# Optimization experiments

Measured on AMD Instinct MI355X. Metric: run time of the kernel, lower is better.

## Reference

```python
import jax, jax.numpy as jnp
import numpy as np

B, H, N, DH = 4096, 4, 1024, 256  # batch, heads, codes per head, per-head dim
DECAY, EPS, COMMIT = 0.99, 1e-5, 0.25


def setup_inputs() -> dict:
    key = jax.random.key(0)
    k1, k2, k3, k4 = jax.random.split(key, 4)
    return {
        "inputs": jax.random.normal(k1, (B, 1, H * DH), dtype=jnp.float32),
        "emb_w": jax.random.normal(k2, (H, N, DH), dtype=jnp.float32),
        "ema_w": jax.random.normal(k3, (H, N, DH), dtype=jnp.float32),
        "cluster_size": jnp.zeros((H, N), dtype=jnp.float32),
        "trans_w": jax.random.normal(k4, (H, N, N), dtype=jnp.float32) * 0.03,
    }


def reference(inputs, emb_w, ema_w, cluster_size, trans_w):
    sg = jax.lax.stop_gradient
    x = inputs[:, 0, :].reshape(B, H, DH)  # split heads
    quant, codes = [], []
    prev_probs = None
    for h in range(H):
        xi = x[:, h]                       # [B, DH]
        w = emb_w[h]                       # [N, DH]
        # squared euclidean distances [B, N]
        d = (jnp.sum(xi * xi, axis=1, keepdims=True)
             + jnp.sum(w * w, axis=1)
             - 2.0 * xi @ w.T)
        logits = -sg(d)
        if prev_probs is not None:  # transition prior from previous head (detached)
            logits = logits + sg(prev_probs @ trans_w[h].T)
        probs = jax.nn.softmax(logits, axis=-1)
        prev_probs = probs
        # EMA codebook update (training mode)
        cs = cluster_size[h] * DECAY + (1.0 - DECAY) * jnp.sum(probs, axis=0)
        n = jnp.sum(cs)
        cs = (cs + EPS) / (n + N * EPS) * n
        dw = probs.T @ xi                  # [N, DH]
        ew = ema_w[h] * DECAY + (1.0 - DECAY) * dw
        new_w = ew / cs[:, None]           # updated codebook used for quantization
        codes.append(jnp.argmax(probs, axis=-1))
        quant.append(probs @ sg(new_w))    # soft-EM quantization, detached codebook
    quantized = jnp.stack(quant, axis=1).reshape(inputs.shape)  # [B,1,H*DH]
    q_loss = jnp.mean((quantized - sg(inputs)) ** 2, axis=(-1, -2))
    e_loss = jnp.mean((sg(quantized) - inputs) ** 2, axis=(-1, -2))
    loss = COMMIT * e_loss + q_loss        # [B]
    quantized = inputs + sg(quantized - inputs)  # straight-through
    vq_codes = jnp.stack(codes, axis=1)    # [B, H]
    return loss, quantized, vq_codes
```

## Files before the change

### kernel.cpp

```cpp
#include <hip/hip_runtime.h>
#include <hip/hip_bf16.h>
#include <math.h>

#define BB 4096
#define HH 4
#define NN 1024
#define DHD 256
#define XLD 1024
#define DECAY 0.99f
#define OMD 0.01f
#define EPSV 1e-5f

typedef __attribute__((ext_vector_type(8))) short bf16x8;
typedef __attribute__((ext_vector_type(4))) float f32x4;
typedef unsigned short u16;

#define MFMA(a, b, c) __builtin_amdgcn_mfma_f32_16x16x32_bf16((a), (b), (c), 0, 0, 0)

static __device__ __forceinline__ u16 f2bf(float x) {
    union { __hip_bfloat16 b; u16 u; } c; c.b = __float2bfloat16(x); return c.u;
}
static __device__ __forceinline__ float bf2f(u16 u) {
    union { __hip_bfloat16 b; u16 u; } c; c.u = u; return __bfloat162float(c.b);
}
static __device__ __forceinline__ void split3(float x, u16& h, u16& m, u16& l) {
    h = f2bf(x);
    float r = x - bf2f(h);
    m = f2bf(r);
    float r2 = r - bf2f(m);
    l = f2bf(r2);
}

__global__ __launch_bounds__(256) void k_prep_x(const float* __restrict__ in,
        u16* __restrict__ xh2, u16* __restrict__ xm2, u16* __restrict__ xl2,
        u16* __restrict__ xth, u16* __restrict__ xtl) {
    __shared__ float T[64][68];
    const int t = threadIdx.x;
    const int c0 = blockIdx.x * 64, i0 = blockIdx.y * 64;
#pragma unroll
    for (int rep = 0; rep < 4; rep++) {
        int id = t + 256 * rep;
        int row = id >> 4, c4 = (id & 15) * 4;
        float4 v = *(const float4*)(in + (size_t)(i0 + row) * XLD + c0 + c4);
        *(float4*)&T[row][c4] = v;
        float xs[4] = {v.x, v.y, v.z, v.w};
        u16 h4[4], m4[4], l4[4];
#pragma unroll
        for (int e = 0; e < 4; e++) split3(2.f * xs[e], h4[e], m4[e], l4[e]);
        size_t o = (size_t)(i0 + row) * XLD + c0 + c4;
        *(ushort4*)(xh2 + o) = make_ushort4(h4[0], h4[1], h4[2], h4[3]);
        *(ushort4*)(xm2 + o) = make_ushort4(m4[0], m4[1], m4[2], m4[3]);
        *(ushort4*)(xl2 + o) = make_ushort4(l4[0], l4[1], l4[2], l4[3]);
    }
    __syncthreads();
    const int or_ = t >> 2, oc = (t & 3) * 16;
    bf16x8 h0, h1, l0, l1;
#pragma unroll
    for (int e = 0; e < 8; e++) {
        float x = T[oc + e][or_];
        u16 h = f2bf(x);
        h0[e] = (short)h; l0[e] = (short)f2bf(x - bf2f(h));
    }
#pragma unroll
    for (int e = 0; e < 8; e++) {
        float x = T[oc + 8 + e][or_];
        u16 h = f2bf(x);
        h1[e] = (short)h; l1[e] = (short)f2bf(x - bf2f(h));
    }
    size_t o = (size_t)(c0 + or_) * BB + i0 + oc;
    *(bf16x8*)(xth + o) = h0;
    *(bf16x8*)(xth + o + 8) = h1;
    *(bf16x8*)(xtl + o) = l0;
    *(bf16x8*)(xtl + o + 8) = l1;
}

__global__ __launch_bounds__(256) void k_prep_w(const float* __restrict__ w,
        u16* __restrict__ wh, u16* __restrict__ wm, u16* __restrict__ wl) {
    size_t id = ((size_t)blockIdx.x * 256 + threadIdx.x) * 4;
    float4 v = *(const float4*)(w + id);
    float xs[4] = {v.x, v.y, v.z, v.w};
    u16 h4[4], m4[4], l4[4];
#pragma unroll
    for (int e = 0; e < 4; e++) split3(xs[e], h4[e], m4[e], l4[e]);
    *(ushort4*)(wh + id) = make_ushort4(h4[0], h4[1], h4[2], h4[3]);
    *(ushort4*)(wm + id) = make_ushort4(m4[0], m4[1], m4[2], m4[3]);
    *(ushort4*)(wl + id) = make_ushort4(l4[0], l4[1], l4[2], l4[3]);
}

__global__ __launch_bounds__(256) void k_prep_t(const float* __restrict__ w,
        u16* __restrict__ th, u16* __restrict__ tl) {
    size_t id = ((size_t)blockIdx.x * 256 + threadIdx.x) * 4;
    float4 v = *(const float4*)(w + id);
    float xs[4] = {v.x, v.y, v.z, v.w};
    u16 h4[4], l4[4];
#pragma unroll
    for (int e = 0; e < 4; e++) {
        u16 h = f2bf(xs[e]);
        h4[e] = h;
        l4[e] = f2bf(xs[e] - bf2f(h));
    }
    *(ushort4*)(th + id) = make_ushort4(h4[0], h4[1], h4[2], h4[3]);
    *(ushort4*)(tl + id) = make_ushort4(l4[0], l4[1], l4[2], l4[3]);
}

__global__ __launch_bounds__(256) void k_wsq(const float* __restrict__ emb,
                                             float* __restrict__ wsq) {
    int wave = threadIdx.x >> 6;
    int lane = threadIdx.x & 63;
    int row  = blockIdx.x * 4 + wave;
    const float* w = emb + (size_t)row * DHD;
    float4 v = *(const float4*)(w + lane * 4);
    float s = v.x * v.x + v.y * v.y + v.z * v.z + v.w * v.w;
    for (int off = 32; off; off >>= 1) s += __shfl_down(s, off);
    if (lane == 0) wsq[row] = s;
}

template <int HASPREV>
__global__ __launch_bounds__(256) void k_logits_mfma(
        const u16* __restrict__ Xh, const u16* __restrict__ Xm, const u16* __restrict__ Xl,
        const u16* __restrict__ Wh, const u16* __restrict__ Wm, const u16* __restrict__ Wl,
        const float* __restrict__ wsq,
        const u16* __restrict__ Ph, const u16* __restrict__ Pl,
        const u16* __restrict__ Th, const u16* __restrict__ Tl,
        float* __restrict__ L) {
    __shared__ u16 Ah[64 * 40], Am[64 * 40], Al[64 * 40];
    __shared__ u16 Bh[64 * 40], Bm[64 * 40], Bl[64 * 40];
    const int t = threadIdx.x;
    const int lane = t & 63, wid = t >> 6;
    const int wmi = wid >> 1, wn = wid & 1;
    const int q = lane >> 4, mr = lane & 15;
    const int j0 = blockIdx.x * 64, i0 = blockIdx.y * 64;
    const int ar = t >> 2, ac = (t & 3) * 8;

    f32x4 zero = {0.f, 0.f, 0.f, 0.f};
    f32x4 s[2][2], acc2[2][2];
#pragma unroll
    for (int mt = 0; mt < 2; mt++)
#pragma unroll
        for (int nt = 0; nt < 2; nt++) { s[mt][nt] = zero; acc2[mt][nt] = zero; }

    for (int kb = 0; kb < DHD; kb += 32) {
        bf16x8 a0h = *(const bf16x8*)(Xh + (size_t)(i0 + ar) * XLD + kb + ac);
        bf16x8 a0m = *(const bf16x8*)(Xm + (size_t)(i0 + ar) * XLD + kb + ac);
        bf16x8 a0l = *(const bf16x8*)(Xl + (size_t)(i0 + ar) * XLD + kb + ac);
        bf16x8 b0h = *(const bf16x8*)(Wh + (size_t)(j0 + ar) * DHD + kb + ac);
        bf16x8 b0m = *(const bf16x8*)(Wm + (size_t)(j0 + ar) * DHD + kb + ac);
        bf16x8 b0l = *(const bf16x8*)(Wl + (size_t)(j0 + ar) * DHD + kb + ac);
        __syncthreads();
        *(bf16x8*)&Ah[ar * 40 + ac] = a0h;
        *(bf16x8*)&Am[ar * 40 + ac] = a0m;
        *(bf16x8*)&Al[ar * 40 + ac] = a0l;
        *(bf16x8*)&Bh[ar * 40 + ac] = b0h;
        *(bf16x8*)&Bm[ar * 40 + ac] = b0m;
        *(bf16x8*)&Bl[ar * 40 + ac] = b0l;
        __syncthreads();
        bf16x8 afh[2], afm[2], afl[2], bfh[2], bfm[2], bfl[2];
#pragma unroll
        for (int mt = 0; mt < 2; mt++) {
            int row = (wmi * 32 + mt * 16 + mr) * 40 + q * 8;
            afh[mt] = *(const bf16x8*)&Ah[row];
            afm[mt] = *(const bf16x8*)&Am[row];
            afl[mt] = *(const bf16x8*)&Al[row];
        }
#pragma unroll
        for (int nt = 0; nt < 2; nt++) {
            int row = (wn * 32 + nt * 16 + mr) * 40 + q * 8;
            bfh[nt] = *(const bf16x8*)&Bh[row];
            bfm[nt] = *(const bf16x8*)&Bm[row];
            bfl[nt] = *(const bf16x8*)&Bl[row];
        }
#pragma unroll
        for (int mt = 0; mt < 2; mt++)
#pragma unroll
            for (int nt = 0; nt < 2; nt++) {
                f32x4 fresh = MFMA(afh[mt], bfh[nt], zero);
                s[mt][nt] += fresh;
                acc2[mt][nt] = MFMA(afh[mt], bfm[nt], acc2[mt][nt]);
                acc2[mt][nt] = MFMA(afm[mt], bfh[nt], acc2[mt][nt]);
                acc2[mt][nt] = MFMA(afh[mt], bfl[nt], acc2[mt][nt]);
                acc2[mt][nt] = MFMA(afm[mt], bfm[nt], acc2[mt][nt]);
                acc2[mt][nt] = MFMA(afl[mt], bfh[nt], acc2[mt][nt]);
            }
    }

    if (HASPREV) {
        for (int kb = 0; kb < NN; kb += 32) {
            bf16x8 a0h = *(const bf16x8*)(Ph + (size_t)(i0 + ar) * NN + kb + ac);
            bf16x8 a0l = *(const bf16x8*)(Pl + (size_t)(i0 + ar) * NN + kb + ac);
            bf16x8 b0h = *(const bf16x8*)(Th + (size_t)(j0 + ar) * NN + kb + ac);
            bf16x8 b0l = *(const bf16x8*)(Tl + (size_t)(j0 + ar) * NN + kb + ac);
            __syncthreads();
            *(bf16x8*)&Ah[ar * 40 + ac] = a0h;
            *(bf16x8*)&Al[ar * 40 + ac] = a0l;
            *(bf16x8*)&Bh[ar * 40 + ac] = b0h;
            *(bf16x8*)&Bl[ar * 40 + ac] = b0l;
            __syncthreads();
            bf16x8 afh[2], afl[2], bfh[2], bfl[2];
#pragma unroll
            for (int mt = 0; mt < 2; mt++) {
                int row = (wmi * 32 + mt * 16 + mr) * 40 + q * 8;
                afh[mt] = *(const bf16x8*)&Ah[row];
                afl[mt] = *(const bf16x8*)&Al[row];
            }
#pragma unroll
            for (int nt = 0; nt < 2; nt++) {
                int row = (wn * 32 + nt * 16 + mr) * 40 + q * 8;
                bfh[nt] = *(const bf16x8*)&Bh[row];
                bfl[nt] = *(const bf16x8*)&Bl[row];
            }
#pragma unroll
            for (int mt = 0; mt < 2; mt++)
#pragma unroll
                for (int nt = 0; nt < 2; nt++) {
                    acc2[mt][nt] = MFMA(afh[mt], bfh[nt], acc2[mt][nt]);
                    acc2[mt][nt] = MFMA(afh[mt], bfl[nt], acc2[mt][nt]);
                    acc2[mt][nt] = MFMA(afl[mt], bfh[nt], acc2[mt][nt]);
                }
        }
    }

    float wq[2];
#pragma unroll
    for (int nt = 0; nt < 2; nt++) wq[nt] = wsq[j0 + wn * 32 + nt * 16 + mr];
#pragma unroll
    for (int mt = 0; mt < 2; mt++)
#pragma unroll
        for (int nt = 0; nt < 2; nt++)
#pragma unroll
            for (int r = 0; r < 4; r++) {
                int gi = i0 + wmi * 32 + mt * 16 + q * 4 + r;
                int gj = j0 + wn * 32 + nt * 16 + mr;
// ... 42 lines not shown
    for (int ss = 128; ss; ss >>= 1) {
        if (t < ss) smax[t] += smax[t + ss];
        __syncthreads();
    }
    float inv = 1.0f / smax[0];
#pragma unroll
    for (int q4 = 0; q4 < 4; q4++) {
        float pv = v[q4] * inv;
        u16 hb = f2bf(pv);
        Ph[(size_t)i * NN + q4 * 256 + t] = hb;
        Pl[(size_t)i * NN + q4 * 256 + t] = f2bf(pv - bf2f(hb));
    }
    if (t == 0) codes[(size_t)i * HH + h] = (float)code;
}

__global__ __launch_bounds__(256) void k_transposeP(const u16* __restrict__ Ph,
        const u16* __restrict__ Pl, u16* __restrict__ PTh, u16* __restrict__ PTl) {
    __shared__ u16 U[64][72];
    const int t = threadIdx.x;
    const int j0 = blockIdx.x * 64, i0 = blockIdx.y * 64;
    for (int pass = 0; pass < 2; pass++) {
        const u16* src = pass ? Pl : Ph;
        u16* dst = pass ? PTl : PTh;
        if (pass) __syncthreads();
#pragma unroll
        for (int rep = 0; rep < 2; rep++) {
            int id = t + 256 * rep;
            int row = id >> 3, c8 = (id & 7) * 8;
            *(bf16x8*)&U[row][c8] = *(const bf16x8*)(src + (size_t)(i0 + row) * NN + j0 + c8);
        }
        __syncthreads();
        int or_ = t >> 2, oc = (t & 3) * 16;
        bf16x8 v0, v1;
#pragma unroll
        for (int e = 0; e < 8; e++) v0[e] = (short)U[oc + e][or_];
#pragma unroll
        for (int e = 0; e < 8; e++) v1[e] = (short)U[oc + 8 + e][or_];
        size_t o = (size_t)(j0 + or_) * BB + i0 + oc;
        *(bf16x8*)(dst + o) = v0;
        *(bf16x8*)(dst + o + 8) = v1;
    }
}

__global__ __launch_bounds__(256) void k_colsum(const u16* __restrict__ Ph,
                                                const u16* __restrict__ Pl,
                                                float* __restrict__ colsum) {
    int j  = blockIdx.x * 256 + threadIdx.x;
    int i0 = blockIdx.y * 256;
    float s = 0.f;
    for (int i = i0; i < i0 + 256; i++)
        s += bf2f(Ph[(size_t)i * NN + j]) + bf2f(Pl[(size_t)i * NN + j]);
    atomicAdd(&colsum[j], s);
}

__global__ __launch_bounds__(1024) void k_cs(const float* __restrict__ cluster_size,
                                             const float* __restrict__ colsum,
                                             float* __restrict__ csn, int h) {
    __shared__ float red[1024];
    int j = threadIdx.x;
    float cs = cluster_size[h * NN + j] * DECAY + OMD * colsum[j];
    red[j] = cs;
    __syncthreads();
    for (int s = 512; s; s >>= 1) {
        if (j < s) red[j] += red[j + s];
        __syncthreads();
    }
    float n = red[0];
    csn[j] = (cs + EPSV) / (n + NN * EPSV) * n;
}

__global__ __launch_bounds__(256) void k_dw(
        const u16* __restrict__ PTh, const u16* __restrict__ PTl,
        const u16* __restrict__ XTh, const u16* __restrict__ XTl,
        float* __restrict__ partial) {
    __shared__ u16 Ah[64 * 40], Al[64 * 40], Bh[64 * 40], Bl[64 * 40];
    const int t = threadIdx.x;
    const int lane = t & 63, wid = t >> 6;
    const int wmi = wid >> 1, wn = wid & 1;
    const int q = lane >> 4, mr = lane & 15;
    const int kd0 = blockIdx.x * 64, j0 = blockIdx.y * 64;
    const int ibeg = blockIdx.z * 256;
    const int ar = t >> 2, ac = (t & 3) * 8;

    f32x4 zero = {0.f, 0.f, 0.f, 0.f};
    f32x4 acc[2][2];
#pragma unroll
    for (int mt = 0; mt < 2; mt++)
#pragma unroll
        for (int nt = 0; nt < 2; nt++) acc[mt][nt] = zero;

    for (int ib = ibeg; ib < ibeg + 256; ib += 32) {
        bf16x8 a0h = *(const bf16x8*)(PTh + (size_t)(j0 + ar) * BB + ib + ac);
        bf16x8 a0l = *(const bf16x8*)(PTl + (size_t)(j0 + ar) * BB + ib + ac);
        bf16x8 b0h = *(const bf16x8*)(XTh + (size_t)(kd0 + ar) * BB + ib + ac);
        bf16x8 b0l = *(const bf16x8*)(XTl + (size_t)(kd0 + ar) * BB + ib + ac);
        __syncthreads();
        *(bf16x8*)&Ah[ar * 40 + ac] = a0h;
        *(bf16x8*)&Al[ar * 40 + ac] = a0l;
        *(bf16x8*)&Bh[ar * 40 + ac] = b0h;
        *(bf16x8*)&Bl[ar * 40 + ac] = b0l;
        __syncthreads();
        bf16x8 afh[2], afl[2], bfh[2], bfl[2];
#pragma unroll
        for (int mt = 0; mt < 2; mt++) {
            int row = (wmi * 32 + mt * 16 + mr) * 40 + q * 8;
            afh[mt] = *(const bf16x8*)&Ah[row];
            afl[mt] = *(const bf16x8*)&Al[row];
        }
#pragma unroll
        for (int nt = 0; nt < 2; nt++) {
            int row = (wn * 32 + nt * 16 + mr) * 40 + q * 8;
            bfh[nt] = *(const bf16x8*)&Bh[row];
            bfl[nt] = *(const bf16x8*)&Bl[row];
        }
#pragma unroll
        for (int mt = 0; mt < 2; mt++)
#pragma unroll
            for (int nt = 0; nt < 2; nt++) {
                acc[mt][nt] = MFMA(afh[mt], bfh[nt], acc[mt][nt]);
                acc[mt][nt] = MFMA(afh[mt], bfl[nt], acc[mt][nt]);
                acc[mt][nt] = MFMA(afl[mt], bfh[nt], acc[mt][nt]);
            }
    }
#pragma unroll
    for (int mt = 0; mt < 2; mt++)
#pragma unroll
        for (int nt = 0; nt < 2; nt++)
#pragma unroll
            for (int r = 0; r < 4; r++) {
                int gj = j0 + wmi * 32 + mt * 16 + q * 4 + r;
                int gk = kd0 + wn * 32 + nt * 16 + mr;
                atomicAdd(&partial[(size_t)gj * DHD + gk], acc[mt][nt][r]);
            }
}

__global__ __launch_bounds__(256) void k_neww_ep(const float* __restrict__ partial,
        const float* __restrict__ ema, const float* __restrict__ csn,
        u16* __restrict__ NWh, u16* __restrict__ NWl) {
    __shared__ float T[64][68];
    const int t = threadIdx.x;
    const int j0 = blockIdx.x * 64, kd0 = blockIdx.y * 64;
#pragma unroll
    for (int rep = 0; rep < 4; rep++) {
        int id = t + 256 * rep;
        int jr = id >> 4, c4 = (id & 15) * 4;
        float4 pp = *(const float4*)(partial + (size_t)(j0 + jr) * DHD + kd0 + c4);
        float4 ee = *(const float4*)(ema + (size_t)(j0 + jr) * DHD + kd0 + c4);
        float ic = 1.0f / csn[j0 + jr];
        float4 v;
        v.x = (ee.x * DECAY + OMD * pp.x) * ic;
        v.y = (ee.y * DECAY + OMD * pp.y) * ic;
        v.z = (ee.z * DECAY + OMD * pp.z) * ic;
        v.w = (ee.w * DECAY + OMD * pp.w) * ic;
        *(float4*)&T[jr][c4] = v;
    }
    __syncthreads();
    const int or_ = t >> 2, oc = (t & 3) * 16;
    bf16x8 h0, h1, l0, l1;
#pragma unroll
    for (int e = 0; e < 8; e++) {
        float x = T[oc + e][or_];
        u16 h = f2bf(x);
        h0[e] = (short)h; l0[e] = (short)f2bf(x - bf2f(h));
    }
#pragma unroll
    for (int e = 0; e < 8; e++) {
        float x = T[oc + 8 + e][or_];
        u16 h = f2bf(x);
        h1[e] = (short)h; l1[e] = (short)f2bf(x - bf2f(h));
    }
    size_t o = (size_t)(kd0 + or_) * NN + j0 + oc;
    *(bf16x8*)(NWh + o) = h0;
    *(bf16x8*)(NWh + o + 8) = h1;
    *(bf16x8*)(NWl + o) = l0;
    *(bf16x8*)(NWl + o + 8) = l1;
}

__global__ __launch_bounds__(256) void k_quant(
        const u16* __restrict__ Ph, const u16* __restrict__ Pl,
        const u16* __restrict__ NWh, const u16* __restrict__ NWl,
        float* __restrict__ outq, int h) {
    __shared__ u16 Ah[64 * 40], Al[64 * 40], Bh[64 * 40], Bl[64 * 40];
    const int t = threadIdx.x;
    const int lane = t & 63, wid = t >> 6;
    const int wmi = wid >> 1, wn = wid & 1;
    const int q = lane >> 4, mr = lane & 15;
    const int kd0 = blockIdx.x * 64, i0 = blockIdx.y * 64;
    const int jbeg = blockIdx.z * 256;
    const int ar = t >> 2, ac = (t & 3) * 8;

    f32x4 zero = {0.f, 0.f, 0.f, 0.f};
    f32x4 acc[2][2];
#pragma unroll
    for (int mt = 0; mt < 2; mt++)
#pragma unroll
        for (int nt = 0; nt < 2; nt++) acc[mt][nt] = zero;

    for (int jb = jbeg; jb < jbeg + 256; jb += 32) {
        bf16x8 a0h = *(const bf16x8*)(Ph + (size_t)(i0 + ar) * NN + jb + ac);
        bf16x8 a0l = *(const bf16x8*)(Pl + (size_t)(i0 + ar) * NN + jb + ac);
        bf16x8 b0h = *(const bf16x8*)(NWh + (size_t)(kd0 + ar) * NN + jb + ac);
        bf16x8 b0l = *(const bf16x8*)(NWl + (size_t)(kd0 + ar) * NN + jb + ac);
        __syncthreads();
        *(bf16x8*)&Ah[ar * 40 + ac] = a0h;
        *(bf16x8*)&Al[ar * 40 + ac] = a0l;
        *(bf16x8*)&Bh[ar * 40 + ac] = b0h;
        *(bf16x8*)&Bl[ar * 40 + ac] = b0l;
        __syncthreads();
        bf16x8 afh[2], afl[2], bfh[2], bfl[2];
#pragma unroll
        for (int mt = 0; mt < 2; mt++) {
            int row = (wmi * 32 + mt * 16 + mr) * 40 + q * 8;
            afh[mt] = *(const bf16x8*)&Ah[row];
            afl[mt] = *(const bf16x8*)&Al[row];
        }
#pragma unroll
        for (int nt = 0; nt < 2; nt++) {
            int row = (wn * 32 + nt * 16 + mr) * 40 + q * 8;
            bfh[nt] = *(const bf16x8*)&Bh[row];
            bfl[nt] = *(const bf16x8*)&Bl[row];
        }
#pragma unroll
        for (int mt = 0; mt < 2; mt++)
#pragma unroll
            for (int nt = 0; nt < 2; nt++) {
                acc[mt][nt] = MFMA(afh[mt], bfh[nt], acc[mt][nt]);
                acc[mt][nt] = MFMA(afh[mt], bfl[nt], acc[mt][nt]);
                acc[mt][nt] = MFMA(afl[mt], bfh[nt], acc[mt][nt]);
            }
    }
#pragma unroll
    for (int mt = 0; mt < 2; mt++)
#pragma unroll
        for (int nt = 0; nt < 2; nt++)
#pragma unroll
            for (int r = 0; r < 4; r++) {
                int gi = i0 + wmi * 32 + mt * 16 + q * 4 + r;
                int gk = kd0 + wn * 32 + nt * 16 + mr;
                atomicAdd(&outq[(size_t)gi * XLD + h * DHD + gk], acc[mt][nt][r]);
            }
}

__global__ __launch_bounds__(256) void k_loss(const float* __restrict__ x,
// ... 23 lines not shown
                              void* d_out, int out_size, void* d_ws, size_t ws_size,
                              hipStream_t stream) {
    const float* inputs = (const float*)d_in[0];
    const float* emb    = (const float*)d_in[1];
    const float* ema    = (const float*)d_in[2];
    const float* csz    = (const float*)d_in[3];
    const float* trans  = (const float*)d_in[4];

    float* out   = (float*)d_out;
    float* loss  = out;
    float* quant = out + BB;
    float* codes = out + BB + (size_t)BB * XLD;

    char* p = (char*)d_ws;
    float* L = (float*)p; p += (size_t)BB * NN * 4;
    u16* PTh = (u16*)L;
    u16* PTl = PTh + (size_t)BB * NN;
    u16* Ph  = (u16*)p; p += (size_t)BB * NN * 2;
    u16* Pl  = (u16*)p; p += (size_t)BB * NN * 2;
    u16* Xh2 = (u16*)p; p += (size_t)BB * XLD * 2;
    u16* Xm2 = (u16*)p; p += (size_t)BB * XLD * 2;
    u16* Xl2 = (u16*)p; p += (size_t)BB * XLD * 2;
    u16* XTh = (u16*)p; p += (size_t)XLD * BB * 2;
    u16* XTl = (u16*)p; p += (size_t)XLD * BB * 2;
    u16* Wh  = (u16*)p; p += (size_t)HH * NN * DHD * 2;
    u16* Wm  = (u16*)p; p += (size_t)HH * NN * DHD * 2;
    u16* Wl  = (u16*)p; p += (size_t)HH * NN * DHD * 2;
    u16* Th  = (u16*)p; p += (size_t)HH * NN * NN * 2;
    u16* Tl  = (u16*)p; p += (size_t)HH * NN * NN * 2;
    u16* NWh = (u16*)p; p += (size_t)DHD * NN * 2;
    u16* NWl = (u16*)p; p += (size_t)DHD * NN * 2;
    float* wsq    = (float*)p; p += (size_t)HH * NN * 4;
    float* colsum = (float*)p; p += NN * 4;
    float* csn    = (float*)p; p += NN * 4;
    float* partial = (float*)p; p += (size_t)NN * DHD * 4;

    k_prep_x<<<dim3(XLD / 64, BB / 64), 256, 0, stream>>>(inputs, Xh2, Xm2, Xl2, XTh, XTl);
    k_prep_w<<<HH * NN * DHD / 1024, 256, 0, stream>>>(emb, Wh, Wm, Wl);
    k_prep_t<<<HH * NN * NN / 1024, 256, 0, stream>>>(trans, Th, Tl);
    k_wsq<<<HH * NN / 4, 256, 0, stream>>>(emb, wsq);
    hipMemsetAsync(quant, 0, (size_t)BB * XLD * 4, stream);

    for (int h = 0; h < HH; h++) {
        const u16* Xhh = Xh2 + h * DHD;
        const u16* Xmh = Xm2 + h * DHD;
        const u16* Xlh = Xl2 + h * DHD;
        const u16* Whh = Wh + (size_t)h * NN * DHD;
        const u16* Wmh = Wm + (size_t)h * NN * DHD;
        const u16* Wlh = Wl + (size_t)h * NN * DHD;
        if (h == 0)
            k_logits_mfma<0><<<dim3(NN / 64, BB / 64), 256, 0, stream>>>(
                Xhh, Xmh, Xlh, Whh, Wmh, Wlh, wsq + h * NN,
                nullptr, nullptr, nullptr, nullptr, L);
        else
            k_logits_mfma<1><<<dim3(NN / 64, BB / 64), 256, 0, stream>>>(
                Xhh, Xmh, Xlh, Whh, Wmh, Wlh, wsq + h * NN,
                Ph, Pl, Th + (size_t)h * NN * NN, Tl + (size_t)h * NN * NN, L);

        k_softmax<<<BB, 256, 0, stream>>>(L, Ph, Pl, codes, h);
        k_transposeP<<<dim3(NN / 64, BB / 64), 256, 0, stream>>>(Ph, Pl, PTh, PTl);

        hipMemsetAsync(colsum, 0, NN * sizeof(float), stream);
        k_colsum<<<dim3(NN / 256, 16), 256, 0, stream>>>(Ph, Pl, colsum);
        k_cs<<<1, NN, 0, stream>>>(csz, colsum, csn, h);

        hipMemsetAsync(partial, 0, (size_t)NN * DHD * sizeof(float), stream);
        k_dw<<<dim3(DHD / 64, NN / 64, 16), 256, 0, stream>>>(
            PTh, PTl, XTh + (size_t)h * DHD * BB, XTl + (size_t)h * DHD * BB, partial);
        k_neww_ep<<<dim3(NN / 64, DHD / 64), 256, 0, stream>>>(
            partial, ema + (size_t)h * NN * DHD, csn, NWh, NWl);

        k_quant<<<dim3(DHD / 64, BB / 64, 4), 256, 0, stream>>>(
            Ph, Pl, NWh, NWl, quant, h);
    }

    k_loss<<<BB, 256, 0, stream>>>(inputs, quant, loss);
}
```

Baseline: 689.0 us.

## Pre-pack GEMM operands into MFMA fragment layout and drop LDS staging

All split-precision operands (X, W, T, P, P^T, new codebook) are written in a fragment-major layout matching the 16x16x32 MFMA register layout. The GEMM kernels then load fragments straight from global memory into registers, with no shared-memory staging and no __syncthreads. This removes LDS round trips and barriers. In exchange it adds an extra pack pass over P each head, and each wave reloads fragments from global/L2 without sharing them across waves in the block.

```diff
diff --git a/kernel.cpp b/kernel.cpp
--- a/kernel.cpp
+++ b/kernel.cpp
@@ -17,6 +17,7 @@
 
 #define MFMA(a, b, c) __builtin_amdgcn_mfma_f32_16x16x32_bf16((a), (b), (c), 0, 0, 0)
 
+
 static __device__ __forceinline__ u16 f2bf(float x) {
     union { __hip_bfloat16 b; u16 u; } c; c.b = __float2bfloat16(x); return c.u;
 }
@@ -32,75 +33,89 @@
 }
 
 __global__ __launch_bounds__(256) void k_prep_x(const float* __restrict__ in,
-        u16* __restrict__ xh2, u16* __restrict__ xm2, u16* __restrict__ xl2,
-        u16* __restrict__ xth, u16* __restrict__ xtl) {
+        u16* __restrict__ xph, u16* __restrict__ xpm, u16* __restrict__ xpl,
+        u16* __restrict__ xtph, u16* __restrict__ xtpl) {
     __shared__ float T[64][68];
-    const int t = threadIdx.x;
+    const int t = threadIdx.x, lane = t & 63, wid = t >> 6;
+    const int q = lane >> 4, mr = lane & 15;
     const int c0 = blockIdx.x * 64, i0 = blockIdx.y * 64;
+    const int h = c0 >> 8, kl0 = c0 & 255;
 #pragma unroll
     for (int rep = 0; rep < 4; rep++) {
         int id = t + 256 * rep;
         int row = id >> 4, c4 = (id & 15) * 4;
         float4 v = *(const float4*)(in + (size_t)(i0 + row) * XLD + c0 + c4);
         *(float4*)&T[row][c4] = v;
-        float xs[4] = {v.x, v.y, v.z, v.w};
-        u16 h4[4], m4[4], l4[4];
-#pragma unroll
-        for (int e = 0; e < 4; e++) split3(2.f * xs[e], h4[e], m4[e], l4[e]);
-        size_t o = (size_t)(i0 + row) * XLD + c0 + c4;
-        *(ushort4*)(xh2 + o) = make_ushort4(h4[0], h4[1], h4[2], h4[3]);
-        *(ushort4*)(xm2 + o) = make_ushort4(m4[0], m4[1], m4[2], m4[3]);
-        *(ushort4*)(xl2 + o) = make_ushort4(l4[0], l4[1], l4[2], l4[3]);
     }
     __syncthreads();
-    const int or_ = t >> 2, oc = (t & 3) * 16;
-    bf16x8 h0, h1, l0, l1;
+    for (int f = wid; f < 8; f += 4) {
+        int a = f >> 1, b = f & 1;
+        bf16x8 vh, vm, vl;
+#pragma unroll
+        for (int e = 0; e < 8; e++) {
+            float x2 = 2.f * T[16 * a + mr][b * 32 + q * 8 + e];
+            u16 hh, mm, ll; split3(x2, hh, mm, ll);
+            vh[e] = (short)hh; vm[e] = (short)mm; vl[e] = (short)ll;
+        }
+        size_t o = (size_t)h * BB * DHD +
+                   ((size_t)((i0 >> 4) + a) * 8 + ((kl0 >> 5) + b)) * 512 + lane * 8;
+        *(bf16x8*)(xph + o) = vh;
+        *(bf16x8*)(xpm + o) = vm;
+        *(bf16x8*)(xpl + o) = vl;
+    }
+    for (int f = wid; f < 8; f += 4) {
+        int a = f >> 1, b = f & 1;
+        bf16x8 vh, vl;
+#pragma unroll
+        for (int e = 0; e < 8; e++) {
+            float x = T[b * 32 + q * 8 + e][16 * a + mr];
+            u16 hh = f2bf(x);
+            u16 ll = f2bf(x - bf2f(hh));
+            vh[e] = (short)hh; vl[e] = (short)ll;
+        }
+        size_t o = (size_t)h * DHD * BB +
+                   ((size_t)((kl0 >> 4) + a) * 128 + ((i0 >> 5) + b)) * 512 + lane * 8;
+        *(bf16x8*)(xtph + o) = vh;
+        *(bf16x8*)(xtpl + o) = vl;
+    }
+}
+
+__global__ __launch_bounds__(256) void k_prep_w(const float* __restrict__ w,
+        u16* __restrict__ wph, u16* __restrict__ wpm, u16* __restrict__ wpl) {
+    const int t = threadIdx.x, lane = t & 63, wid = t >> 6;
+    const int q = lane >> 4, mr = lane & 15;
+    int fid = blockIdx.x * 4 + wid;
+    int kt = fid & 7, jt = (fid >> 3) & 63, h = fid >> 9;
+    const float* src = w + (size_t)(h * NN + jt * 16 + mr) * DHD + kt * 32 + q * 8;
+    bf16x8 vh, vm, vl;
 #pragma unroll
     for (int e = 0; e < 8; e++) {
-        float x = T[oc + e][or_];
-        u16 h = f2bf(x);
-        h0[e] = (short)h; l0[e] = (short)f2bf(x - bf2f(h));
-    }
+        u16 hh, mm, ll; split3(src[e], hh, mm, ll);
+        vh[e] = (short)hh; vm[e] = (short)mm; vl[e] = (short)ll;
+    }
+    size_t o = (size_t)h * NN * DHD + ((size_t)jt * 8 + kt) * 512 + lane * 8;
+    *(bf16x8*)(wph + o) = vh;
+    *(bf16x8*)(wpm + o) = vm;
+    *(bf16x8*)(wpl + o) = vl;
+}
+
+__global__ __launch_bounds__(256) void k_prep_t(const float* __restrict__ w,
+        u16* __restrict__ tph, u16* __restrict__ tpl) {
+    const int t = threadIdx.x, lane = t & 63, wid = t >> 6;
+    const int q = lane >> 4, mr = lane & 15;
+    int fid = blockIdx.x * 4 + wid;
+    int kt = fid & 31, jt = (fid >> 5) & 63, h = fid >> 11;
+    const float* src = w + (size_t)(h * NN + jt * 16 + mr) * NN + kt * 32 + q * 8;
+    bf16x8 vh, vl;
 #pragma unroll
     for (int e = 0; e < 8; e++) {
-        float x = T[oc + 8 + e][or_];
-        u16 h = f2bf(x);
-        h1[e] = (short)h; l1[e] = (short)f2bf(x - bf2f(h));
-    }
-    size_t o = (size_t)(c0 + or_) * BB + i0 + oc;
-    *(bf16x8*)(xth + o) = h0;
-    *(bf16x8*)(xth + o + 8) = h1;
-    *(bf16x8*)(xtl + o) = l0;
-    *(bf16x8*)(xtl + o + 8) = l1;
-}
-
-__global__ __launch_bounds__(256) void k_prep_w(const float* __restrict__ w,
-        u16* __restrict__ wh, u16* __restrict__ wm, u16* __restrict__ wl) {
-    size_t id = ((size_t)blockIdx.x * 256 + threadIdx.x) * 4;
-    float4 v = *(const float4*)(w + id);
-    float xs[4] = {v.x, v.y, v.z, v.w};
-    u16 h4[4], m4[4], l4[4];
-#pragma unroll
-    for (int e = 0; e < 4; e++) split3(xs[e], h4[e], m4[e], l4[e]);
-    *(ushort4*)(wh + id) = make_ushort4(h4[0], h4[1], h4[2], h4[3]);
-    *(ushort4*)(wm + id) = make_ushort4(m4[0], m4[1], m4[2], m4[3]);
-    *(ushort4*)(wl + id) = make_ushort4(l4[0], l4[1], l4[2], l4[3]);
-}
-
-__global__ __launch_bounds__(256) void k_prep_t(const float* __restrict__ w,
-        u16* __restrict__ th, u16* __restrict__ tl) {
-    size_t id = ((size_t)blockIdx.x * 256 + threadIdx.x) * 4;
-    float4 v = *(const float4*)(w + id);
-    float xs[4] = {v.x, v.y, v.z, v.w};
-    u16 h4[4], l4[4];
-#pragma unroll
-    for (int e = 0; e < 4; e++) {
-        u16 h = f2bf(xs[e]);
-        h4[e] = h;
-        l4[e] = f2bf(xs[e] - bf2f(h));
-    }
-    *(ushort4*)(th + id) = make_ushort4(h4[0], h4[1], h4[2], h4[3]);
-    *(ushort4*)(tl + id) = make_ushort4(l4[0], l4[1], l4[2], l4[3]);
+        u16 hh = f2bf(src[e]);
+        u16 ll = f2bf(src[e] - bf2f(hh));
+        vh[e] = (short)hh; vl[e] = (short)ll;
+    }
+    size_t o = (size_t)h * NN * NN + ((size_t)jt * 32 + kt) * 512 + lane * 8;
+    *(bf16x8*)(tph + o) = vh;
+    *(bf16x8*)(tpl + o) = vl;
 }
 
 __global__ __launch_bounds__(256) void k_wsq(const float* __restrict__ emb,
@@ -116,21 +131,21 @@
 }
 
 template <int HASPREV>
-__global__ __launch_bounds__(256) void k_logits_mfma(
-        const u16* __restrict__ Xh, const u16* __restrict__ Xm, const u16* __restrict__ Xl,
-        const u16* __restrict__ Wh, const u16* __restrict__ Wm, const u16* __restrict__ Wl,
+__global__ __launch_bounds__(256) void k_logits_frag(
+        const u16* __restrict__ Xph, const u16* __restrict__ Xpm, const u16* __restrict__ Xpl,
+        const u16* __restrict__ Wph, const u16* __restrict__ Wpm, const u16* __restrict__ Wpl,
         const float* __restrict__ wsq,
-        const u16* __restrict__ Ph, const u16* __restrict__ Pl,
-        const u16* __restrict__ Th, const u16* __restrict__ Tl,
+        const u16* __restrict__ Pph, const u16* __restrict__ Ppl,
+        const u16* __restrict__ Tph, const u16* __restrict__ Tpl,
         float* __restrict__ L) {
-    __shared__ u16 Ah[64 * 40], Am[64 * 40], Al[64 * 40];
-    __shared__ u16 Bh[64 * 40], Bm[64 * 40], Bl[64 * 40];
     const int t = threadIdx.x;
     const int lane = t & 63, wid = t >> 6;
     const int wmi = wid >> 1, wn = wid & 1;
     const int q = lane >> 4, mr = lane & 15;
     const int j0 = blockIdx.x * 64, i0 = blockIdx.y * 64;
-    const int ar = t >> 2, ac = (t & 3) * 8;
+    const int it0 = (i0 >> 4) + wmi * 2;
+    const int jt0 = (j0 >> 4) + wn * 2;
+    const int lo = lane * 8;
 
     f32x4 zero = {0.f, 0.f, 0.f, 0.f};
     f32x4 s[2][2], acc2[2][2];
@@ -139,82 +154,80 @@
 #pragma unroll
         for (int nt = 0; nt < 2; nt++) { s[mt][nt] = zero; acc2[mt][nt] = zero; }
 
-    for (int kb = 0; kb < DHD; kb += 32) {
-        bf16x8 a0h = *(const bf16x8*)(Xh + (size_t)(i0 + ar) * XLD + kb + ac);
-        bf16x8 a0m = *(const bf16x8*)(Xm + (size_t)(i0 + ar) * XLD + kb + ac);
-        bf16x8 a0l = *(const bf16x8*)(Xl + (size_t)(i0 + ar) * XLD + kb + ac);
-        bf16x8 b0h = *(const bf16x8*)(Wh + (size_t)(j0 + ar) * DHD + kb + ac);
-        bf16x8 b0m = *(const bf16x8*)(Wm + (size_t)(j0 + ar) * DHD + kb + ac);
-        bf16x8 b0l = *(const bf16x8*)(Wl + (size_t)(j0 + ar) * DHD + kb + ac);
-        __syncthreads();
-        *(bf16x8*)&Ah[ar * 40 + ac] = a0h;
-        *(bf16x8*)&Am[ar * 40 + ac] = a0m;
-        *(bf16x8*)&Al[ar * 40 + ac] = a0l;
-        *(bf16x8*)&Bh[ar * 40 + ac] = b0h;
-        *(bf16x8*)&Bm[ar * 40 + ac] = b0m;
-        *(bf16x8*)&Bl[ar * 40 + ac] = b0l;
-        __syncthreads();
-        bf16x8 afh[2], afm[2], afl[2], bfh[2], bfm[2], bfl[2];
+    {
+        const u16 *ahp[2], *amp[2], *alp[2], *bhp[2], *bmp[2], *blp[2];
 #pragma unroll
         for (int mt = 0; mt < 2; mt++) {
-            int row = (wmi * 32 + mt * 16 + mr) * 40 + q * 8;
-            afh[mt] = *(const bf16x8*)&Ah[row];
-            afm[mt] = *(const bf16x8*)&Am[row];
-            afl[mt] = *(const bf16x8*)&Al[row];
+            size_t b = (size_t)(it0 + mt) * 8 * 512 + lo;
+            ahp[mt] = Xph + b; amp[mt] = Xpm + b; alp[mt] = Xpl + b;
         }
 #pragma unroll
         for (int nt = 0; nt < 2; nt++) {
-            int row = (wn * 32 + nt * 16 + mr) * 40 + q * 8;
-            bfh[nt] = *(const bf16x8*)&Bh[row];
-            bfm[nt] = *(const bf16x8*)&Bm[row];
-            bfl[nt] = *(const bf16x8*)&Bl[row];
-        }
-#pragma unroll
-        for (int mt = 0; mt < 2; mt++)
+            size_t b = (size_t)(jt0 + nt) * 8 * 512 + lo;
+            bhp[nt] = Wph + b; bmp[nt] = Wpm + b; blp[nt] = Wpl + b;
+        }
+#pragma unroll 2
+        for (int kt = 0; kt < 8; kt++) {
+            bf16x8 ah[2], am[2], al[2], bh[2], bm[2], bl[2];
+#pragma unroll
+            for (int mt = 0; mt < 2; mt++) {
+                ah[mt] = *(const bf16x8*)(ahp[mt] + kt * 512);
+                am[mt] = *(const bf16x8*)(amp[mt] + kt * 512);
+                al[mt] = *(const bf16x8*)(alp[mt] + kt * 512);
+            }
 #pragma unroll
             for (int nt = 0; nt < 2; nt++) {
-                f32x4 fresh = MFMA(afh[mt], bfh[nt], zero);
-                s[mt][nt] += fresh;
-                acc2[mt][nt] = MFMA(afh[mt], bfm[nt], acc2[mt][nt]);
-                acc2[mt][nt] = MFMA(afm[mt], bfh[nt], acc2[mt][nt]);
-                acc2[mt][nt] = MFMA(afh[mt], bfl[nt], acc2[mt][nt]);
-                acc2[mt][nt] = MFMA(afm[mt], bfm[nt], acc2[mt][nt]);
-                acc2[mt][nt] = MFMA(afl[mt], bfh[nt], acc2[mt][nt]);
-            }
+                bh[nt] = *(const bf16x8*)(bhp[nt] + kt * 512);
+                bm[nt] = *(const bf16x8*)(bmp[nt] + kt * 512);
+                bl[nt] = *(const bf16x8*)(blp[nt] + kt * 512);
+            }
+#pragma unroll
+            for (int mt = 0; mt < 2; mt++)
+#pragma unroll
+                for (int nt = 0; nt < 2; nt++) {
+                    f32x4 fresh = MFMA(ah[mt], bh[nt], zero);
+                    s[mt][nt] += fresh;
+                    acc2[mt][nt] = MFMA(ah[mt], bm[nt], acc2[mt][nt]);
+                    acc2[mt][nt] = MFMA(am[mt], bh[nt], acc2[mt][nt]);
+                    acc2[mt][nt] = MFMA(ah[mt], bl[nt], acc2[mt][nt]);
+                    acc2[mt][nt] = MFMA(am[mt], bm[nt], acc2[mt][nt]);
+                    acc2[mt][nt] = MFMA(al[mt], bh[nt], acc2[mt][nt]);
+                }
+        }
     }
 
     if (HASPREV) {
-        for (int kb = 0; kb < NN; kb += 32) {
-            bf16x8 a0h = *(const bf16x8*)(Ph + (size_t)(i0 + ar) * NN + kb + ac);
-            bf16x8 a0l = *(const bf16x8*)(Pl + (size_t)(i0 + ar) * NN + kb + ac);
-            bf16x8 b0h = *(const bf16x8*)(Th + (size_t)(j0 + ar) * NN + kb + ac);
-            bf16x8 b0l = *(const bf16x8*)(Tl + (size_t)(j0 + ar) * NN + kb + ac);
-            __syncthreads();
-            *(bf16x8*)&Ah[ar * 40 + ac] = a0h;
-            *(bf16x8*)&Al[ar * 40 + ac] = a0l;
-            *(bf16x8*)&Bh[ar * 40 + ac] = b0h;
-            *(bf16x8*)&Bl[ar * 40 + ac] = b0l;
-            __syncthreads();
-            bf16x8 afh[2], afl[2], bfh[2], bfl[2];
+        const u16 *ahp[2], *alp[2], *bhp[2], *blp[2];
+#pragma unroll
+        for (int mt = 0; mt < 2; mt++) {
+            size_t b = (size_t)(it0 + mt) * 32 * 512 + lo;
+            ahp[mt] = Pph + b; alp[mt] = Ppl + b;
+        }
+#pragma unroll
+        for (int nt = 0; nt < 2; nt++) {
+            size_t b = (size_t)(jt0 + nt) * 32 * 512 + lo;
+            bhp[nt] = Tph + b; blp[nt] = Tpl + b;
+        }
+#pragma unroll 2
+        for (int kt = 0; kt < 32; kt++) {
+            bf16x8 ah[2], al[2], bh[2], bl[2];
 #pragma unroll
             for (int mt = 0; mt < 2; mt++) {
-                int row = (wmi * 32 + mt * 16 + mr) * 40 + q * 8;
-                afh[mt] = *(const bf16x8*)&Ah[row];
-                afl[mt] = *(const bf16x8*)&Al[row];
+                ah[mt] = *(const bf16x8*)(ahp[mt] + kt * 512);
+                al[mt] = *(const bf16x8*)(alp[mt] + kt * 512);
             }
 #pragma unroll
             for (int nt = 0; nt < 2; nt++) {
-                int row = (wn * 32 + nt * 16 + mr) * 40 + q * 8;
-                bfh[nt] = *(const bf16x8*)&Bh[row];
-                bfl[nt] = *(const bf16x8*)&Bl[row];
+                bh[nt] = *(const bf16x8*)(bhp[nt] + kt * 512);
+                bl[nt] = *(const bf16x8*)(blp[nt] + kt * 512);
             }
 #pragma unroll
             for (int mt = 0; mt < 2; mt++)
 #pragma unroll
                 for (int nt = 0; nt < 2; nt++) {
-                    acc2[mt][nt] = MFMA(afh[mt], bfh[nt], acc2[mt][nt]);
-                    acc2[mt][nt] = MFMA(afh[mt], bfl[nt], acc2[mt][nt]);
-                    acc2[mt][nt] = MFMA(afl[mt], bfh[nt], acc2[mt][nt]);
+                    acc2[mt][nt] = MFMA(ah[mt], bh[nt], acc2[mt][nt]);
+                    acc2[mt][nt] = MFMA(ah[mt], bl[nt], acc2[mt][nt]);
+                    acc2[mt][nt] = MFMA(al[mt], bh[nt], acc2[mt][nt]);
                 }
         }
     }
@@ -287,14 +300,29 @@
     if (t == 0) codes[(size_t)i * HH + h] = (float)code;
 }
 
-__global__ __launch_bounds__(256) void k_transposeP(const u16* __restrict__ Ph,
-        const u16* __restrict__ Pl, u16* __restrict__ PTh, u16* __restrict__ PTl) {
+__global__ __launch_bounds__(256) void k_packP(const u16* __restrict__ Ph,
+        const u16* __restrict__ Pl, u16* __restrict__ Pph, u16* __restrict__ Ppl) {
+    const int t = threadIdx.x, lane = t & 63, wid = t >> 6;
+    const int q = lane >> 4, mr = lane & 15;
+    int fid = blockIdx.x * 4 + wid;
+    int kt = fid & 31, it = fid >> 5;
+    size_t si = (size_t)(it * 16 + mr) * NN + kt * 32 + q * 8;
+    bf16x8 vh = *(const bf16x8*)(Ph + si);
+    bf16x8 vl = *(const bf16x8*)(Pl + si);
+    size_t o = ((size_t)it * 32 + kt) * 512 + lane * 8;
+    *(bf16x8*)(Pph + o) = vh;
+    *(bf16x8*)(Ppl + o) = vl;
+}
+
+__global__ __launch_bounds__(256) void k_packPT(const u16* __restrict__ Ph,
+        const u16* __restrict__ Pl, u16* __restrict__ PTph, u16* __restrict__ PTpl) {
     __shared__ u16 U[64][72];
-    const int t = threadIdx.x;
+    const int t = threadIdx.x, lane = t & 63, wid = t >> 6;
+    const int q = lane >> 4, mr = lane & 15;
     const int j0 = blockIdx.x * 64, i0 = blockIdx.y * 64;
     for (int pass = 0; pass < 2; pass++) {
         const u16* src = pass ? Pl : Ph;
-        u16* dst = pass ? PTl : PTh;
+        u16* dst = pass ? PTpl : PTph;
         if (pass) __syncthreads();
 #pragma unroll
         for (int rep = 0; rep < 2; rep++) {
@@ -303,15 +331,14 @@
             *(bf16x8*)&U[row][c8] = *(const bf16x8*)(src + (size_t)(i0 + row) * NN + j0 + c8);
         }
         __syncthreads();
-        int or_ = t >> 2, oc = (t & 3) * 16;
-        bf16x8 v0, v1;
-#pragma unroll
-        for (int e = 0; e < 8; e++) v0[e] = (short)U[oc + e][or_];
-#pragma unroll
-        for (int e = 0; e < 8; e++) v1[e] = (short)U[oc + 8 + e][or_];
-        size_t o = (size_t)(j0 + or_) * BB + i0 + oc;
-        *(bf16x8*)(dst + o) = v0;
-        *(bf16x8*)(dst + o + 8) = v1;
+        for (int f = wid; f < 8; f += 4) {
+            int a = f >> 1, b = f & 1;
+            bf16x8 v;
+#pragma unroll
+            for (int e = 0; e < 8; e++) v[e] = (short)U[b * 32 + q * 8 + e][16 * a + mr];
+            size_t o = ((size_t)((j0 >> 4) + a) * 128 + ((i0 >> 5) + b)) * 512 + lane * 8;
+            *(bf16x8*)(dst + o) = v;
+        }
     }
 }
 
@@ -342,18 +369,19 @@
     csn[j] = (cs + EPSV) / (n + NN * EPSV) * n;
 }
 
-__global__ __launch_bounds__(256) void k_dw(
-        const u16* __restrict__ PTh, const u16* __restrict__ PTl,
-        const u16* __restrict__ XTh, const u16* __restrict__ XTl,
+__global__ __launch_bounds__(256) void k_dw_frag(
+        const u16* __restrict__ PTph, const u16* __restrict__ PTpl,
+        const u16* __restrict__ XTph, const u16* __restrict__ XTpl,
         float* __restrict__ partial) {
-    __shared__ u16 Ah[64 * 40], Al[64 * 40], Bh[64 * 40], Bl[64 * 40];
     const int t = threadIdx.x;
     const int lane = t & 63, wid = t >> 6;
     const int wmi = wid >> 1, wn = wid & 1;
     const int q = lane >> 4, mr = lane & 15;
     const int kd0 = blockIdx.x * 64, j0 = blockIdx.y * 64;
-    const int ibeg = blockIdx.z * 256;
-    const int ar = t >> 2, ac = (t & 3) * 8;
+    const int z = blockIdx.z;
+    const int jt0 = (j0 >> 4) + wmi * 2;
+    const int kdt0 = (kd0 >> 4) + wn * 2;
+    const int lo = lane * 8;
 
     f32x4 zero = {0.f, 0.f, 0.f, 0.f};
     f32x4 acc[2][2];
@@ -362,37 +390,37 @@
 #pragma unroll
         for (int nt = 0; nt < 2; nt++) acc[mt][nt] = zero;
 
-    for (int ib = ibeg; ib < ibeg + 256; ib += 32) {
-        bf16x8 a0h = *(const bf16x8*)(PTh + (size_t)(j0 + ar) * BB + ib + ac);
-        bf16x8 a0l = *(const bf16x8*)(PTl + (size_t)(j0 + ar) * BB + ib + ac);
-        bf16x8 b0h = *(const bf16x8*)(XTh + (size_t)(kd0 + ar) * BB + ib + ac);
-        bf16x8 b0l = *(const bf16x8*)(XTl + (size_t)(kd0 + ar) * BB + ib + ac);
-        __syncthreads();
-        *(bf16x8*)&Ah[ar * 40 + ac] = a0h;
-        *(bf16x8*)&Al[ar * 40 + ac] = a0l;
-        *(bf16x8*)&Bh[ar * 40 + ac] = b0h;
-        *(bf16x8*)&Bl[ar * 40 + ac] = b0l;
-        __syncthreads();
-        bf16x8 afh[2], afl[2], bfh[2], bfl[2];
+    const u16 *ahp[2], *alp[2], *bhp[2], *blp[2];
+#pragma unroll
+    for (int mt = 0; mt < 2; mt++) {
+        size_t b = ((size_t)(jt0 + mt) * 128 + z * 8) * 512 + lo;
+        ahp[mt] = PTph + b; alp[mt] = PTpl + b;
+    }
+#pragma unroll
+    for (int nt = 0; nt < 2; nt++) {
+        size_t b = ((size_t)(kdt0 + nt) * 128 + z * 8) * 512 + lo;
+        bhp[nt] = XTph + b; blp[nt] = XTpl + b;
+    }
+#pragma unroll 2
+    for (int kt = 0; kt < 8; kt++) {
+        bf16x8 ah[2], al[2], bh[2], bl[2];
 #pragma unroll
         for (int mt = 0; mt < 2; mt++) {
-            int row = (wmi * 32 + mt * 16 + mr) * 40 + q * 8;
-            afh[mt] = *(const bf16x8*)&Ah[row];
-            afl[mt] = *(const bf16x8*)&Al[row];
+            ah[mt] = *(const bf16x8*)(ahp[mt] + kt * 512);
+            al[mt] = *(const bf16x8*)(alp[mt] + kt * 512);
         }
 #pragma unroll
         for (int nt = 0; nt < 2; nt++) {
-            int row = (wn * 32 + nt * 16 + mr) * 40 + q * 8;
-            bfh[nt] = *(const bf16x8*)&Bh[row];
-            bfl[nt] = *(const bf16x8*)&Bl[row];
+            bh[nt] = *(const bf16x8*)(bhp[nt] + kt * 512);
+            bl[nt] = *(const bf16x8*)(blp[nt] + kt * 512);
         }
 #pragma unroll
         for (int mt = 0; mt < 2; mt++)
 #pragma unroll
             for (int nt = 0; nt < 2; nt++) {
-                acc[mt][nt] = MFMA(afh[mt], bfh[nt], acc[mt][nt]);
-                acc[mt][nt] = MFMA(afh[mt], bfl[nt], acc[mt][nt]);
-                acc[mt][nt] = MFMA(afl[mt], bfh[nt], acc[mt][nt]);
+                acc[mt][nt] = MFMA(ah[mt], bh[nt], acc[mt][nt]);
+                acc[mt][nt] = MFMA(ah[mt], bl[nt], acc[mt][nt]);
+                acc[mt][nt] = MFMA(al[mt], bh[nt], acc[mt][nt]);
             }
     }
 #pragma unroll
@@ -409,9 +437,10 @@
 
 __global__ __launch_bounds__(256) void k_neww_ep(const float* __restrict__ partial,
         const float* __restrict__ ema, const float* __restrict__ csn,
-        u16* __restrict__ NWh, u16* __restrict__ NWl) {
+        u16* __restrict__ NWph, u16* __restrict__ NWpl) {
     __shared__ float T[64][68];
-    const int t = threadIdx.x;
+    const int t = threadIdx.x, lane = t & 63, wid = t >> 6;
+    const int q = lane >> 4, mr = lane & 15;
     const int j0 = blockIdx.x * 64, kd0 = blockIdx.y * 64;
 #pragma unroll
     for (int rep = 0; rep < 4; rep++) {
@@ -428,39 +457,35 @@
         *(float4*)&T[jr][c4] = v;
     }
     __syncthreads();
-    const int or_ = t >> 2, oc = (t & 3) * 16;
-    bf16x8 h0, h1, l0, l1;
-#pragma unroll
-    for (int e = 0; e < 8; e++) {
-        float x = T[oc + e][or_];
-        u16 h = f2bf(x);
-        h0[e] = (short)h; l0[e] = (short)f2bf(x - bf2f(h));
-    }
-#pragma unroll
-    for (int e = 0; e < 8; e++) {
-        float x = T[oc + 8 + e][or_];
-        u16 h = f2bf(x);
-        h1[e] = (short)h; l1[e] = (short)f2bf(x - bf2f(h));
-    }
-    size_t o = (size_t)(kd0 + or_) * NN + j0 + oc;
-    *(bf16x8*)(NWh + o) = h0;
-    *(bf16x8*)(NWh + o + 8) = h1;
-    *(bf16x8*)(NWl + o) = l0;
-    *(bf16x8*)(NWl + o + 8) = l1;
-}
-
-__global__ __launch_bounds__(256) void k_quant(
-        const u16* __restrict__ Ph, const u16* __restrict__ Pl,
-        const u16* __restrict__ NWh, const u16* __restrict__ NWl,
+    for (int f = wid; f < 8; f += 4) {
+        int a = f >> 1, b = f & 1;
+        bf16x8 vh, vl;
+#pragma unroll
+        for (int e = 0; e < 8; e++) {
+            float x = T[b * 32 + q * 8 + e][16 * a + mr];
+            u16 hh = f2bf(x);
+            u16 ll = f2bf(x - bf2f(hh));
+            vh[e] = (short)hh; vl[e] = (short)ll;
+        }
+        size_t o = ((size_t)((kd0 >> 4) + a) * 32 + ((j0 >> 5) + b)) * 512 + lane * 8;
+        *(bf16x8*)(NWph + o) = vh;
+        *(bf16x8*)(NWpl + o) = vl;
+    }
+}
+
+__global__ __launch_bounds__(256) void k_quant_frag(
+        const u16* __restrict__ Pph, const u16* __restrict__ Ppl,
+        const u16* __restrict__ NWph, const u16* __restrict__ NWpl,
         float* __restrict__ outq, int h) {
-    __shared__ u16 Ah[64 * 40], Al[64 * 40], Bh[64 * 40], Bl[64 * 40];
     const int t = threadIdx.x;
     const int lane = t & 63, wid = t >> 6;
     const int wmi = wid >> 1, wn = wid & 1;
     const int q = lane >> 4, mr = lane & 15;
     const int kd0 = blockIdx.x * 64, i0 = blockIdx.y * 64;
-    const int jbeg = blockIdx.z * 256;
-    const int ar = t >> 2, ac = (t & 3) * 8;
+    const int z = blockIdx.z;
+    const int it0 = (i0 >> 4) + wmi * 2;
+    const int kdt0 = (kd0 >> 4) + wn * 2;
+    const int lo = lane * 8;
 
     f32x4 zero = {0.f, 0.f, 0.f, 0.f};
     f32x4 acc[2][2];
@@ -469,37 +494,37 @@
 #pragma unroll
         for (int nt = 0; nt < 2; nt++) acc[mt][nt] = zero;
 
-    for (int jb = jbeg; jb < jbeg + 256; jb += 32) {
-        bf16x8 a0h = *(const bf16x8*)(Ph + (size_t)(i0 + ar) * NN + jb + ac);
-        bf16x8 a0l = *(const bf16x8*)(Pl + (size_t)(i0 + ar) * NN + jb + ac);
-        bf16x8 b0h = *(const bf16x8*)(NWh + (size_t)(kd0 + ar) * NN + jb + ac);
-        bf16x8 b0l = *(const bf16x8*)(NWl + (size_t)(kd0 + ar) * NN + jb + ac);
-        __syncthreads();
-        *(bf16x8*)&Ah[ar * 40 + ac] = a0h;
-        *(bf16x8*)&Al[ar * 40 + ac] = a0l;
-        *(bf16x8*)&Bh[ar * 40 + ac] = b0h;
-        *(bf16x8*)&Bl[ar * 40 + ac] = b0l;
-        __syncthreads();
-        bf16x8 afh[2], afl[2], bfh[2], bfl[2];
+    const u16 *ahp[2], *alp[2], *bhp[2], *blp[2];
+#pragma unroll
+    for (int mt = 0; mt < 2; mt++) {
+        size_t b = ((size_t)(it0 + mt) * 32 + z * 8) * 512 + lo;
+        ahp[mt] = Pph + b; alp[mt] = Ppl + b;
+    }
+#pragma unroll
+    for (int nt = 0; nt < 2; nt++) {
+        size_t b = ((size_t)(kdt0 + nt) * 32 + z * 8) * 512 + lo;
+        bhp[nt] = NWph + b; blp[nt] = NWpl + b;
+    }
+#pragma unroll 2
+    for (int kt = 0; kt < 8; kt++) {
+        bf16x8 ah[2], al[2], bh[2], bl[2];
 #pragma unroll
         for (int mt = 0; mt < 2; mt++) {
-            int row = (wmi * 32 + mt * 16 + mr) * 40 + q * 8;
-            afh[mt] = *(const bf16x8*)&Ah[row];
-            afl[mt] = *(const bf16x8*)&Al[row];
+            ah[mt] = *(const bf16x8*)(ahp[mt] + kt * 512);
+            al[mt] = *(const bf16x8*)(alp[mt] + kt * 512);
         }
 #pragma unroll
         for (int nt = 0; nt < 2; nt++) {
-            int row = (wn * 32 + nt * 16 + mr) * 40 + q * 8;
-            bfh[nt] = *(const bf16x8*)&Bh[row];
-            bfl[nt] = *(const bf16x8*)&Bl[row];
+            bh[nt] = *(const bf16x8*)(bhp[nt] + kt * 512);
+            bl[nt] = *(const bf16x8*)(blp[nt] + kt * 512);
         }
 #pragma unroll
         for (int mt = 0; mt < 2; mt++)
 #pragma unroll
             for (int nt = 0; nt < 2; nt++) {
-                acc[mt][nt] = MFMA(afh[mt], bfh[nt], acc[mt][nt]);
-                acc[mt][nt] = MFMA(afh[mt], bfl[nt], acc[mt][nt]);
-                acc[mt][nt] = MFMA(afl[mt], bfh[nt], acc[mt][nt]);
+                acc[mt][nt] = MFMA(ah[mt], bh[nt], acc[mt][nt]);
+                acc[mt][nt] = MFMA(ah[mt], bl[nt], acc[mt][nt]);
+                acc[mt][nt] = MFMA(al[mt], bh[nt], acc[mt][nt]);
             }
     }
 #pragma unroll
@@ -553,64 +578,67 @@
 
     char* p = (char*)d_ws;
     float* L = (float*)p; p += (size_t)BB * NN * 4;
-    u16* PTh = (u16*)L;
-    u16* PTl = PTh + (size_t)BB * NN;
-    u16* Ph  = (u16*)p; p += (size_t)BB * NN * 2;
-    u16* Pl  = (u16*)p; p += (size_t)BB * NN * 2;
-    u16* Xh2 = (u16*)p; p += (size_t)BB * XLD * 2;
-    u16* Xm2 = (u16*)p; p += (size_t)BB * XLD * 2;
-    u16* Xl2 = (u16*)p; p += (size_t)BB * XLD * 2;
-    u16* XTh = (u16*)p; p += (size_t)XLD * BB * 2;
-    u16* XTl = (u16*)p; p += (size_t)XLD * BB * 2;
-    u16* Wh  = (u16*)p; p += (size_t)HH * NN * DHD * 2;
-    u16* Wm  = (u16*)p; p += (size_t)HH * NN * DHD * 2;
-    u16* Wl  = (u16*)p; p += (size_t)HH * NN * DHD * 2;
-    u16* Th  = (u16*)p; p += (size_t)HH * NN * NN * 2;
-    u16* Tl  = (u16*)p; p += (size_t)HH * NN * NN * 2;
-    u16* NWh = (u16*)p; p += (size_t)DHD * NN * 2;
-    u16* NWl = (u16*)p; p += (size_t)DHD * NN * 2;
+    u16* PTph = (u16*)L;
+    u16* PTpl = PTph + (size_t)BB * NN;
+    u16* Ph   = (u16*)p; p += (size_t)BB * NN * 2;
+    u16* Pl   = (u16*)p; p += (size_t)BB * NN * 2;
+    u16* Pph  = (u16*)p; p += (size_t)BB * NN * 2;
+    u16* Ppl  = (u16*)p; p += (size_t)BB * NN * 2;
+    u16* Xph  = (u16*)p; p += (size_t)BB * XLD * 2;
+    u16* Xpm  = (u16*)p; p += (size_t)BB * XLD * 2;
+    u16* Xpl  = (u16*)p; p += (size_t)BB * XLD * 2;
+    u16* XTph = (u16*)p; p += (size_t)XLD * BB * 2;
+    u16* XTpl = (u16*)p; p += (size_t)XLD * BB * 2;
+    u16* Wph  = (u16*)p; p += (size_t)HH * NN * DHD * 2;
+    u16* Wpm  = (u16*)p; p += (size_t)HH * NN * DHD * 2;
+    u16* Wpl  = (u16*)p; p += (size_t)HH * NN * DHD * 2;
+    u16* Tph  = (u16*)p; p += (size_t)HH * NN * NN * 2;
+    u16* Tpl  = (u16*)p; p += (size_t)HH * NN * NN * 2;
+    u16* NWph = (u16*)p; p += (size_t)DHD * NN * 2;
+    u16* NWpl = (u16*)p; p += (size_t)DHD * NN * 2;
     float* wsq    = (float*)p; p += (size_t)HH * NN * 4;
     float* colsum = (float*)p; p += NN * 4;
     float* csn    = (float*)p; p += NN * 4;
     float* partial = (float*)p; p += (size_t)NN * DHD * 4;
 
-    k_prep_x<<<dim3(XLD / 64, BB / 64), 256, 0, stream>>>(inputs, Xh2, Xm2, Xl2, XTh, XTl);
-    k_prep_w<<<HH * NN * DHD / 1024, 256, 0, stream>>>(emb, Wh, Wm, Wl);
-    k_prep_t<<<HH * NN * NN / 1024, 256, 0, stream>>>(trans, Th, Tl);
+    k_prep_x<<<dim3(XLD / 64, BB / 64), 256, 0, stream>>>(inputs, Xph, Xpm, Xpl, XTph, XTpl);
+    k_prep_w<<<HH * 64 * 8 / 4, 256, 0, stream>>>(emb, Wph, Wpm, Wpl);
+    k_prep_t<<<HH * 64 * 32 / 4, 256, 0, stream>>>(trans, Tph, Tpl);
     k_wsq<<<HH * NN / 4, 256, 0, stream>>>(emb, wsq);
     hipMemsetAsync(quant, 0, (size_t)BB * XLD * 4, stream);
 
     for (int h = 0; h < HH; h++) {
-        const u16* Xhh = Xh2 + h * DHD;
-        const u16* Xmh = Xm2 + h * DHD;
-        const u16* Xlh = Xl2 + h * DHD;
-        const u16* Whh = Wh + (size_t)h * NN * DHD;
-        const u16* Wmh = Wm + (size_t)h * NN * DHD;
-        const u16* Wlh = Wl + (size_t)h * NN * DHD;
+        const u16* Xhh = Xph + (size_t)h * BB * DHD;
+        const u16* Xmh = Xpm + (size_t)h * BB * DHD;
+        const u16* Xlh = Xpl + (size_t)h * BB * DHD;
+        const u16* Whh = Wph + (size_t)h * NN * DHD;
+        const u16* Wmh = Wpm + (size_t)h * NN * DHD;
+        const u16* Wlh = Wpl + (size_t)h * NN * DHD;
         if (h == 0)
-            k_logits_mfma<0><<<dim3(NN / 64, BB / 64), 256, 0, stream>>>(
+            k_logits_frag<0><<<dim3(NN / 64, BB / 64), 256, 0, stream>>>(
                 Xhh, Xmh, Xlh, Whh, Wmh, Wlh, wsq + h * NN,
                 nullptr, nullptr, nullptr, nullptr, L);
         else
-            k_logits_mfma<1><<<dim3(NN / 64, BB / 64), 256, 0, stream>>>(
+            k_logits_frag<1><<<dim3(NN / 64, BB / 64), 256, 0, stream>>>(
                 Xhh, Xmh, Xlh, Whh, Wmh, Wlh, wsq + h * NN,
-                Ph, Pl, Th + (size_t)h * NN * NN, Tl + (size_t)h * NN * NN, L);
+                Pph, Ppl, Tph + (size_t)h * NN * NN, Tpl + (size_t)h * NN * NN, L);
 
         k_softmax<<<BB, 256, 0, stream>>>(L, Ph, Pl, codes, h);
-        k_transposeP<<<dim3(NN / 64, BB / 64), 256, 0, stream>>>(Ph, Pl, PTh, PTl);
+        k_packP<<<BB / 16 * NN / 32 / 4, 256, 0, stream>>>(Ph, Pl, Pph, Ppl);
+        k_packPT<<<dim3(NN / 64, BB / 64), 256, 0, stream>>>(Ph, Pl, PTph, PTpl);
 
         hipMemsetAsync(colsum, 0, NN * sizeof(float), stream);
         k_colsum<<<dim3(NN / 256, 16), 256, 0, stream>>>(Ph, Pl, colsum);
         k_cs<<<1, NN, 0, stream>>>(csz, colsum, csn, h);
 
         hipMemsetAsync(partial, 0, (size_t)NN * DHD * sizeof(float), stream);
-        k_dw<<<dim3(DHD / 64, NN / 64, 16), 256, 0, stream>>>(
-            PTh, PTl, XTh + (size_t)h * DHD * BB, XTl + (size_t)h * DHD * BB, partial);
+        k_dw_frag<<<dim3(DHD / 64, NN / 64, 16), 256, 0, stream>>>(
+            PTph, PTpl, XTph + (size_t)h * DHD * BB, XTpl + (size_t)h * DHD * BB, partial);
         k_neww_ep<<<dim3(NN / 64, DHD / 64), 256, 0, stream>>>(
-            partial, ema + (size_t)h * NN * DHD, csn, NWh, NWl);
-
-        k_quant<<<dim3(DHD / 64, BB / 64, 4), 256, 0, stream>>>(
-            Ph, Pl, NWh, NWl, quant, h);
+            partial, ema + (size_t)h * NN * DHD, csn, NWph, NWpl);
+
+        k_quant_frag<<<dim3(DHD / 64, BB / 64, 4), 256, 0, stream>>>(
+            Pph, Ppl, NWph, NWpl, quant, h);
     }
 
     k_loss<<<BB, 256, 0, stream>>>(inputs, quant, loss);
```

After: 669.6 us. 1.03x faster.
